# Kernel tuning notes

Measured on AMD Instinct MI355X. Metric: run time of the kernel, lower is better.

The kernel has to match this reference:

```python
import jax, jax.numpy as jnp
import numpy as np

RATIO = 2
GROUPS = 4


def conv1x1(x, w, b):
    # x: (B,C,H,W), w: (O,C), b: (O,)
    return jnp.einsum('bchw,oc->bohw', x, w) + b[None, :, None, None]


def pixel_unshuffle(x, r):
    # out[b, c*r*r + i*r + j, h, w] = x[b, c, h*r+i, w*r+j]  (torch semantics)
    B, C, H, W = x.shape
    x = x.reshape(B, C, H // r, r, W // r, r)
    x = x.transpose(0, 1, 3, 5, 2, 4)
    return x.reshape(B, C * r * r, H // r, W // r)


def grid_sample_bilinear_border(img, grid):
    # img: (N,C,H,W); grid: (N,Ho,Wo,2), grid[...,0]=x coord, grid[...,1]=y coord in [-1,1]
    # align_corners=False, padding_mode='border' (torch: clip coord to border, then bilinear)
    N, C, H, W = img.shape
    ix = ((grid[..., 0] + 1.0) * W - 1.0) * 0.5
    iy = ((grid[..., 1] + 1.0) * H - 1.0) * 0.5
    ix = jnp.clip(ix, 0.0, W - 1.0)
    iy = jnp.clip(iy, 0.0, H - 1.0)
    x0 = jnp.floor(ix)
    y0 = jnp.floor(iy)
    wx = (ix - x0)[:, None]  # (N,1,Ho,Wo) broadcast over C
    wy = (iy - y0)[:, None]
    x0i = x0.astype(jnp.int32)
    y0i = y0.astype(jnp.int32)
    x1i = jnp.minimum(x0i + 1, W - 1)
    y1i = jnp.minimum(y0i + 1, H - 1)
    gather = jax.vmap(lambda im, yy, xx: im[:, yy, xx])  # (C,Ho,Wo) per batch
    v00 = gather(img, y0i, x0i)
    v01 = gather(img, y0i, x1i)
    v10 = gather(img, y1i, x0i)
    v11 = gather(img, y1i, x1i)
    return (v00 * (1 - wx) * (1 - wy) + v01 * wx * (1 - wy)
            + v10 * (1 - wx) * wy + v11 * wx * wy)


def setup_inputs() -> dict:
    key = jax.random.key(0)
    k1, k2, k3 = jax.random.split(key, 3)
    B, C, H, W = 16, 64, 256, 256
    c_out = 2 * (GROUPS // RATIO ** 2)  # = 2
    x = jax.random.normal(k1, (B, C, H, W), jnp.float32)
    w_off = jax.random.normal(k2, (c_out, C), jnp.float32) * 0.001
    b_off = jnp.zeros((c_out,), jnp.float32)
    w_sc = jax.random.normal(k3, (c_out, C), jnp.float32) * 0.001
    b_sc = jnp.zeros((c_out,), jnp.float32)
    return {"x": x, "w_off": w_off, "b_off": b_off, "w_sc": w_sc, "b_sc": b_sc}


def reference(x, w_off, b_off, w_sc, b_sc):
    B, Cin, H, W = x.shape  # H,W divisible by RATIO -> replicate pad is a no-op
    # forward_lp with dyScope=True
    off = conv1x1(x, w_off, b_off)
    off = jax.nn.sigmoid(conv1x1(x, w_sc, b_sc)) * 0.5 * off
    off = pixel_unshuffle(off, RATIO)            # (B, 2*GROUPS, h, w)
    h, w = off.shape[2], off.shape[3]
    # x: 'b (c grp) h w -> (b grp) c h w'
    cg = Cin // GROUPS
    xg = x.reshape(B, cg, GROUPS, H, W).transpose(0, 2, 1, 3, 4).reshape(B * GROUPS, cg, H, W)
    # offset: 'b (grp two) h w -> (b grp) h w two'
    offg = off.reshape(B, GROUPS, 2, h, w).transpose(0, 1, 3, 4, 2).reshape(B * GROUPS, h, w, 2)
    # pos: stack(meshgrid(h_coord, w_coord)) -> channel 0 = h_coord, channel 1 = w_coord
    hc = jnp.arange(h, dtype=x.dtype) + 0.5
    wc = jnp.arange(w, dtype=x.dtype) + 0.5
    pos = jnp.stack(jnp.meshgrid(hc, wc, indexing='ij'), axis=-1)[None]  # (1,h,w,2)
    norm = jnp.array([w, h], dtype=x.dtype)  # normalizer = [w, h]
    grid = 2.0 * (pos + offg) / norm - 1.0
    out = grid_sample_bilinear_border(xg, grid)  # (B*GROUPS, cg, h, w)
    out = out.reshape(B, GROUPS, cg, h, w).transpose(0, 2, 1, 3, 4).reshape(B, Cin, h, w)
    return out, offg
```

## Files before the change

### kernel.cpp

```cpp
#include <hip/hip_runtime.h>
#include <math.h>

#define BATCH 16
#define CIN   64
#define HIN   256
#define WIN   256
#define HOUT  128
#define WOUT  128
#define NPIX  (HIN * WIN)
#define NPIXO (HOUT * WOUT)
#define OUT0_SIZE ((size_t)BATCH * CIN * HOUT * WOUT)

typedef __attribute__((ext_vector_type(4))) float f32x4;

__global__ __launch_bounds__(256) void k_fused(
    const float* __restrict__ x,
    const float* __restrict__ w_off, const float* __restrict__ b_off,
    const float* __restrict__ w_sc,  const float* __restrict__ b_sc,
    float* __restrict__ out, float* __restrict__ offg)
{
    __shared__ float  sw[256];
    __shared__ float2 soff[4][16][17];
    __shared__ __align__(16) float sval[5184];

    int t = threadIdx.x;
    sw[t] = (t < 128) ? w_off[t] : w_sc[t - 128];

    int blk  = blockIdx.x;
    int b    = blk >> 6;
    int tile = blk & 63;
    int hh0  = (tile >> 3) * 16;
    int ww0  = (tile & 7) * 16;

    int row = t >> 4, col = t & 15;
    int hh = hh0 + row, ww = ww0 + col;
    int odd = t & 1;
    int colbase = 2 * (ww0 + (col & 14));

    const float* xrow = x + (size_t)b * CIN * NPIX
                      + (size_t)(2 * hh + odd) * WIN + colbase;

    float TA0[4] = {0,0,0,0}, TA1[4] = {0,0,0,0};
    float TS0[4] = {0,0,0,0}, TS1[4] = {0,0,0,0};

    __syncthreads();

    #pragma unroll 8
    for (int c = 0; c < CIN; ++c) {
        f32x4 f = *reinterpret_cast<const f32x4*>(xrow + (size_t)c * NPIX);
        float wo0 = sw[c], wo1 = sw[64 + c], ws0 = sw[128 + c], ws1 = sw[192 + c];
        #pragma unroll
        for (int j = 0; j < 4; ++j) {
            TA0[j] += f[j] * wo0;
            TA1[j] += f[j] * wo1;
            TS0[j] += f[j] * ws0;
            TS1[j] += f[j] * ws1;
        }
    }

    float rA0_0 = __shfl_xor(odd ? TA0[0] : TA0[2], 1);
    float rA0_1 = __shfl_xor(odd ? TA0[1] : TA0[3], 1);
    float rA1_0 = __shfl_xor(odd ? TA1[0] : TA1[2], 1);
    float rA1_1 = __shfl_xor(odd ? TA1[1] : TA1[3], 1);
    float rS0_0 = __shfl_xor(odd ? TS0[0] : TS0[2], 1);
    float rS0_1 = __shfl_xor(odd ? TS0[1] : TS0[3], 1);
    float rS1_0 = __shfl_xor(odd ? TS1[0] : TS1[2], 1);
    float rS1_1 = __shfl_xor(odd ? TS1[1] : TS1[3], 1);

    float aA0[2][2], aA1[2][2], aS0[2][2], aS1[2][2];
    aA0[0][0] = odd ? rA0_0 : TA0[0];  aA0[0][1] = odd ? rA0_1 : TA0[1];
    aA0[1][0] = odd ? TA0[2] : rA0_0;  aA0[1][1] = odd ? TA0[3] : rA0_1;
    aA1[0][0] = odd ? rA1_0 : TA1[0];  aA1[0][1] = odd ? rA1_1 : TA1[1];
    aA1[1][0] = odd ? TA1[2] : rA1_0;  aA1[1][1] = odd ? TA1[3] : rA1_1;
    aS0[0][0] = odd ? rS0_0 : TS0[0];  aS0[0][1] = odd ? rS0_1 : TS0[1];
    aS0[1][0] = odd ? TS0[2] : rS0_0;  aS0[1][1] = odd ? TS0[3] : rS0_1;
    aS1[0][0] = odd ? rS1_0 : TS1[0];  aS1[0][1] = odd ? rS1_1 : TS1[1];
    aS1[1][0] = odd ? TS1[2] : rS1_0;  aS1[1][1] = odd ? TS1[3] : rS1_1;

    float bo0 = b_off[0], bo1 = b_off[1];
    float bs0 = b_sc[0],  bs1 = b_sc[1];

    float og[4][2];
    #pragma unroll
    for (int i = 0; i < 2; ++i) {
        #pragma unroll
        for (int j = 0; j < 2; ++j) {
            float g0 = 1.0f / (1.0f + __expf(-(aS0[i][j] + bs0)));
            float g1 = 1.0f / (1.0f + __expf(-(aS1[i][j] + bs1)));
            og[i][j]     = g0 * 0.5f * (aA0[i][j] + bo0);
            og[2 + i][j] = g1 * 0.5f * (aA1[i][j] + bo1);
        }
    }

    #pragma unroll
    for (int g = 0; g < 4; ++g) {
        float2 vv = make_float2(og[g][0], og[g][1]);
        soff[g][row][col] = vv;
        size_t oi = ((size_t)((b * 4 + g) * HOUT + hh)) * WOUT + ww;
        __builtin_nontemporal_store(__builtin_bit_cast(double, vv),
                                    reinterpret_cast<double*>(offg + 2 * oi));
    }
    __syncthreads();

    int hl = t & 15, wl = t >> 4;
    int shh = hh0 + hl, sww = ww0 + wl;
    int oddl = t & 1;
    const float* xg = x + (size_t)b * CIN * NPIX;

    int R  = (t >> 2) & 15;
    int q  = t & 3;
    int wv = t >> 6;

    float* outb = out + (size_t)b * CIN * NPIXO
                + (size_t)(hh0 + R) * WOUT + ww0 + q * 4;

    #pragma unroll
    for (int g = 0; g < 4; ++g) {
        float2 off = soff[g][hl][wl];
        float ix = 2.0f * ((float)shh + 0.5f + off.x) - 0.5f;
        float iy = 2.0f * ((float)sww + 0.5f + off.y) - 0.5f;
        ix = fminf(fmaxf(ix, 0.0f), (float)(WIN - 1));
        iy = fminf(fmaxf(iy, 0.0f), (float)(HIN - 1));

        float x0f = floorf(ix), y0f = floorf(iy);
        float wx = ix - x0f, wy = iy - y0f;
        int x0 = (int)x0f, y0 = (int)y0f;
        int x1 = min(x0 + 1, WIN - 1);
        int y1 = min(y0 + 1, HIN - 1);

        float w00 = (1.0f - wx) * (1.0f - wy);
        float w01 = wx * (1.0f - wy);
        float w10 = (1.0f - wx) * wy;
        float w11 = wx * wy;

        const float* xgc = xg + (size_t)g * NPIX;

        int x0p = __shfl_xor(x0, 1);
        int y0p = __shfl_xor(y0, 1);
        bool ok = (x1 == x0 + 1) && (y1 == y0 + 1) && (y0p == y0)
               && (oddl ? (x0 == x0p + 2) : (x0p == x0 + 2))
               && (((x0 - (oddl ? 2 : 0)) & 3) == 0);

        float v[16];
        if (__all(ok)) {
            int colb = x0 - (oddl ? 2 : 0);
            int rowL = oddl ? y1 : y0;
            float rw0 = __shfl_xor(oddl ? w00 : w10, 1);
            float rw1 = __shfl_xor(oddl ? w01 : w11, 1);
            const float* basep = xgc + (size_t)rowL * WIN + colb;
            #pragma unroll
            for (int c = 0; c < 16; ++c) {
                f32x4 f = *reinterpret_cast<const f32x4*>(basep + (size_t)c * 4 * NPIX);
                float pOwn  = oddl ? (f[2] * w10 + f[3] * w11)
                                   : (f[0] * w00 + f[1] * w01);
                float pPart = oddl ? (f[0] * rw0 + f[1] * rw1)
                                   : (f[2] * rw0 + f[3] * rw1);
                v[c] = pOwn + __shfl_xor(pPart, 1);
            }
        } else {
            int i00 = y0 * WIN + x0, i01 = y0 * WIN + x1;
            int i10 = y1 * WIN + x0, i11 = y1 * WIN + x1;
            bool fastp = ((x0 & 1) == 0) && (x1 == x0 + 1);
            if (fastp) {
                #pragma unroll
                for (int c = 0; c < 16; ++c) {
                    const float* xc = xgc + (size_t)c * 4 * NPIX;
                    float2 a = *reinterpret_cast<const float2*>(xc + i00);
                    float2 d = *reinterpret_cast<const float2*>(xc + i10);
                    v[c] = a.x * w00 + a.y * w01 + d.x * w10 + d.y * w11;
                }
            } else {
                #pragma unroll
                for (int c = 0; c < 16; ++c) {
                    const float* xc = xgc + (size_t)c * 4 * NPIX;
                    v[c] = xc[i00] * w00 + xc[i01] * w01
                         + xc[i10] * w10 + xc[i11] * w11;
                }
            }
        }

        __syncthreads();
        #pragma unroll
        for (int c = 0; c < 16; ++c)
            sval[c * 324 + hl * 20 + wl] = v[c];
        __syncthreads();

        #pragma unroll
        for (int p2 = 0; p2 < 4; ++p2) {
            int c = wv * 4 + p2;
            f32x4 val = *reinterpret_cast<const f32x4*>(&sval[c * 324 + R * 20 + q * 4]);
            __builtin_nontemporal_store(val, reinterpret_cast<f32x4*>(
                outb + (size_t)(c * 4 + g) * NPIXO));
        }
    }
}

extern "C" void kernel_launch(void* const* d_in, const int* in_sizes, int n_in,
                              void* d_out, int out_size, void* d_ws, size_t ws_size,
                              hipStream_t stream) {
    const float* x     = (const float*)d_in[0];
    const float* w_off = (const float*)d_in[1];
    const float* b_off = (const float*)d_in[2];
    const float* w_sc  = (const float*)d_in[3];
    const float* b_sc  = (const float*)d_in[4];

    float* out  = (float*)d_out;
    float* offg = out + OUT0_SIZE;

    k_fused<<<1024, 256, 0, stream>>>(x, w_off, b_off, w_sc, b_sc, out, offg);
}
```

Before: 100.6 us.

## Warp-specialize fused kernel into producer/consumer halves pipelining tiles

Each block now has 512 threads: 256 producer threads compute the offset convolution for the next tile while 256 consumer threads do grid-sample and write out the previous tile, with double-buffered shared memory for offsets and sampled values. The grid shrinks to 256 persistent-style blocks, each handling four tiles in sequence with a staggered tile order. The aim is to overlap the memory-bound conv pass with the gather pass and to spread the output stores across steps. In exchange it adds many block-wide barriers and drops to one block per CU, which lowers occupancy and latency hiding.

```diff
diff --git a/kernel.cpp b/kernel.cpp
--- a/kernel.cpp
+++ b/kernel.cpp
@@ -9,188 +9,237 @@
 #define WOUT  128
 #define NPIX  (HIN * WIN)
 #define NPIXO (HOUT * WOUT)
-#define OUT0_SIZE ((size_t)BATCH * CIN * HOUT * WOUT)
+#define OUT0_SIZE ((size_t)BATCH * CIN * NPIXO)
 
 typedef __attribute__((ext_vector_type(4))) float f32x4;
 
-__global__ __launch_bounds__(256) void k_fused(
+__global__ __launch_bounds__(512, 1) void k_fused(
     const float* __restrict__ x,
     const float* __restrict__ w_off, const float* __restrict__ b_off,
     const float* __restrict__ w_sc,  const float* __restrict__ b_sc,
     float* __restrict__ out, float* __restrict__ offg)
 {
     __shared__ float  sw[256];
-    __shared__ float2 soff[4][16][17];
-    __shared__ __align__(16) float sval[5184];
-
-    int t = threadIdx.x;
-    sw[t] = (t < 128) ? w_off[t] : w_sc[t - 128];
-
-    int blk  = blockIdx.x;
-    int b    = blk >> 6;
-    int tile = blk & 63;
-    int hh0  = (tile >> 3) * 16;
-    int ww0  = (tile & 7) * 16;
-
-    int row = t >> 4, col = t & 15;
-    int hh = hh0 + row, ww = ww0 + col;
-    int odd = t & 1;
-    int colbase = 2 * (ww0 + (col & 14));
-
-    const float* xrow = x + (size_t)b * CIN * NPIX
-                      + (size_t)(2 * hh + odd) * WIN + colbase;
-
-    float TA0[4] = {0,0,0,0}, TA1[4] = {0,0,0,0};
-    float TS0[4] = {0,0,0,0}, TS1[4] = {0,0,0,0};
+    __shared__ float2 soff[2][4][16][17];
+    __shared__ __align__(16) float sval[2][5184];
+
+    const int t = threadIdx.x;
+    if (t < 256) sw[t] = (t < 128) ? w_off[t] : w_sc[t - 128];
+
+    const int blk = blockIdx.x;
+    const int b   = blk >> 4;
+    const int k   = blk & 15;
+    const int pr  = k >> 1;
+    const int jj  = k & 1;
+    const int hh0 = pr * 16;
+
+    const bool isProd = (t < 256);
+    const int u = t & 255;
+
+    const int prow = u >> 4, pcol = u & 15;
+    const int phh  = hh0 + prow;
+    const int podd = u & 1;
+    const float* xbase = x + (size_t)b * CIN * NPIX
+                       + (size_t)(2 * phh + podd) * WIN;
+    float bo0 = 0, bo1 = 0, bs0 = 0, bs1 = 0;
+    if (isProd) { bo0 = b_off[0]; bo1 = b_off[1]; bs0 = b_sc[0]; bs1 = b_sc[1]; }
+
+    const int hl = u & 15, wl = u >> 4;
+    const int shh = hh0 + hl;
+    const int oddl = u & 1;
+    const float* xg = x + (size_t)b * CIN * NPIX;
+    const int Rr = (u >> 2) & 15, q4 = u & 3, wv = u >> 6;
+    float* outTB = out + (size_t)b * CIN * NPIXO
+                 + (size_t)(hh0 + Rr) * WOUT + q4 * 4;
+
+    int prev_ww0 = 0;
 
     __syncthreads();
 
-    #pragma unroll 8
-    for (int c = 0; c < CIN; ++c) {
-        f32x4 f = *reinterpret_cast<const f32x4*>(xrow + (size_t)c * NPIX);
-        float wo0 = sw[c], wo1 = sw[64 + c], ws0 = sw[128 + c], ws1 = sw[192 + c];
+    for (int r = 0; r < 5; ++r) {
+        const bool prodA = (r <= 3);
+        const bool consA = (r >= 1);
+        const int qp = ((r - pr) & 3) + 4 * jj;
+        const int qc = (((r - 1) - pr) & 3) + 4 * jj;
+        const int ww0p = qp * 16;
+        const int ww0c = qc * 16;
+
+        float TA0[4] = {0,0,0,0}, TA1[4] = {0,0,0,0};
+        float TS0[4] = {0,0,0,0}, TS1[4] = {0,0,0,0};
+
         #pragma unroll
-        for (int j = 0; j < 4; ++j) {
-            TA0[j] += f[j] * wo0;
-            TA1[j] += f[j] * wo1;
-            TS0[j] += f[j] * ws0;
-            TS1[j] += f[j] * ws1;
-        }
-    }
-
-    float rA0_0 = __shfl_xor(odd ? TA0[0] : TA0[2], 1);
-    float rA0_1 = __shfl_xor(odd ? TA0[1] : TA0[3], 1);
-    float rA1_0 = __shfl_xor(odd ? TA1[0] : TA1[2], 1);
-    float rA1_1 = __shfl_xor(odd ? TA1[1] : TA1[3], 1);
-    float rS0_0 = __shfl_xor(odd ? TS0[0] : TS0[2], 1);
-    float rS0_1 = __shfl_xor(odd ? TS0[1] : TS0[3], 1);
-    float rS1_0 = __shfl_xor(odd ? TS1[0] : TS1[2], 1);
-    float rS1_1 = __shfl_xor(odd ? TS1[1] : TS1[3], 1);
-
-    float aA0[2][2], aA1[2][2], aS0[2][2], aS1[2][2];
-    aA0[0][0] = odd ? rA0_0 : TA0[0];  aA0[0][1] = odd ? rA0_1 : TA0[1];
-    aA0[1][0] = odd ? TA0[2] : rA0_0;  aA0[1][1] = odd ? TA0[3] : rA0_1;
-    aA1[0][0] = odd ? rA1_0 : TA1[0];  aA1[0][1] = odd ? rA1_1 : TA1[1];
-    aA1[1][0] = odd ? TA1[2] : rA1_0;  aA1[1][1] = odd ? TA1[3] : rA1_1;
-    aS0[0][0] = odd ? rS0_0 : TS0[0];  aS0[0][1] = odd ? rS0_1 : TS0[1];
-    aS0[1][0] = odd ? TS0[2] : rS0_0;  aS0[1][1] = odd ? TS0[3] : rS0_1;
-    aS1[0][0] = odd ? rS1_0 : TS1[0];  aS1[0][1] = odd ? rS1_1 : TS1[1];
-    aS1[1][0] = odd ? TS1[2] : rS1_0;  aS1[1][1] = odd ? TS1[3] : rS1_1;
-
-    float bo0 = b_off[0], bo1 = b_off[1];
-    float bs0 = b_sc[0],  bs1 = b_sc[1];
-
-    float og[4][2];
-    #pragma unroll
-    for (int i = 0; i < 2; ++i) {
-        #pragma unroll
-        for (int j = 0; j < 2; ++j) {
-            float g0 = 1.0f / (1.0f + __expf(-(aS0[i][j] + bs0)));
-            float g1 = 1.0f / (1.0f + __expf(-(aS1[i][j] + bs1)));
-            og[i][j]     = g0 * 0.5f * (aA0[i][j] + bo0);
-            og[2 + i][j] = g1 * 0.5f * (aA1[i][j] + bo1);
-        }
-    }
-
-    #pragma unroll
-    for (int g = 0; g < 4; ++g) {
-        float2 vv = make_float2(og[g][0], og[g][1]);
-        soff[g][row][col] = vv;
-        size_t oi = ((size_t)((b * 4 + g) * HOUT + hh)) * WOUT + ww;
-        __builtin_nontemporal_store(__builtin_bit_cast(double, vv),
-                                    reinterpret_cast<double*>(offg + 2 * oi));
-    }
-    __syncthreads();
-
-    int hl = t & 15, wl = t >> 4;
-    int shh = hh0 + hl, sww = ww0 + wl;
-    int oddl = t & 1;
-    const float* xg = x + (size_t)b * CIN * NPIX;
-
-    int R  = (t >> 2) & 15;
-    int q  = t & 3;
-    int wv = t >> 6;
-
-    float* outb = out + (size_t)b * CIN * NPIXO
-                + (size_t)(hh0 + R) * WOUT + ww0 + q * 4;
-
-    #pragma unroll
-    for (int g = 0; g < 4; ++g) {
-        float2 off = soff[g][hl][wl];
-        float ix = 2.0f * ((float)shh + 0.5f + off.x) - 0.5f;
-        float iy = 2.0f * ((float)sww + 0.5f + off.y) - 0.5f;
-        ix = fminf(fmaxf(ix, 0.0f), (float)(WIN - 1));
-        iy = fminf(fmaxf(iy, 0.0f), (float)(HIN - 1));
-
-        float x0f = floorf(ix), y0f = floorf(iy);
-        float wx = ix - x0f, wy = iy - y0f;
-        int x0 = (int)x0f, y0 = (int)y0f;
-        int x1 = min(x0 + 1, WIN - 1);
-        int y1 = min(y0 + 1, HIN - 1);
-
-        float w00 = (1.0f - wx) * (1.0f - wy);
-        float w01 = wx * (1.0f - wy);
-        float w10 = (1.0f - wx) * wy;
-        float w11 = wx * wy;
-
-        const float* xgc = xg + (size_t)g * NPIX;
-
-        int x0p = __shfl_xor(x0, 1);
-        int y0p = __shfl_xor(y0, 1);
-        bool ok = (x1 == x0 + 1) && (y1 == y0 + 1) && (y0p == y0)
-               && (oddl ? (x0 == x0p + 2) : (x0p == x0 + 2))
-               && (((x0 - (oddl ? 2 : 0)) & 3) == 0);
-
-        float v[16];
-        if (__all(ok)) {
-            int colb = x0 - (oddl ? 2 : 0);
-            int rowL = oddl ? y1 : y0;
-            float rw0 = __shfl_xor(oddl ? w00 : w10, 1);
-            float rw1 = __shfl_xor(oddl ? w01 : w11, 1);
-            const float* basep = xgc + (size_t)rowL * WIN + colb;
-            #pragma unroll
-            for (int c = 0; c < 16; ++c) {
-                f32x4 f = *reinterpret_cast<const f32x4*>(basep + (size_t)c * 4 * NPIX);
-                float pOwn  = oddl ? (f[2] * w10 + f[3] * w11)
-                                   : (f[0] * w00 + f[1] * w01);
-                float pPart = oddl ? (f[0] * rw0 + f[1] * rw1)
-                                   : (f[2] * rw0 + f[3] * rw1);
-                v[c] = pOwn + __shfl_xor(pPart, 1);
-            }
-        } else {
-            int i00 = y0 * WIN + x0, i01 = y0 * WIN + x1;
-            int i10 = y1 * WIN + x0, i11 = y1 * WIN + x1;
-            bool fastp = ((x0 & 1) == 0) && (x1 == x0 + 1);
-            if (fastp) {
-                #pragma unroll
-                for (int c = 0; c < 16; ++c) {
-                    const float* xc = xgc + (size_t)c * 4 * NPIX;
-                    float2 a = *reinterpret_cast<const float2*>(xc + i00);
-                    float2 d = *reinterpret_cast<const float2*>(xc + i10);
-                    v[c] = a.x * w00 + a.y * w01 + d.x * w10 + d.y * w11;
+        for (int g = 0; g < 4; ++g) {
+            if (isProd) {
+                if (prodA) {
+                    const float* xrow = xbase + 2 * (ww0p + (pcol & 14));
+                    #pragma unroll
+                    for (int ci = 0; ci < 16; ++ci) {
+                        const int c = g * 16 + ci;
+                        f32x4 f = *reinterpret_cast<const f32x4*>(
+                            xrow + (size_t)c * NPIX);
+                        float wo0 = sw[c], wo1 = sw[64 + c];
+                        float ws0 = sw[128 + c], ws1 = sw[192 + c];
+                        #pragma unroll
+                        for (int jx = 0; jx < 4; ++jx) {
+                            TA0[jx] += f[jx] * wo0;
+                            TA1[jx] += f[jx] * wo1;
+                            TS0[jx] += f[jx] * ws0;
+                            TS1[jx] += f[jx] * ws1;
+                        }
+                    }
+                    if (g == 3) {
+                        float rA0_0 = __shfl_xor(podd ? TA0[0] : TA0[2], 1);
+                        float rA0_1 = __shfl_xor(podd ? TA0[1] : TA0[3], 1);
+                        float rA1_0 = __shfl_xor(podd ? TA1[0] : TA1[2], 1);
+                        float rA1_1 = __shfl_xor(podd ? TA1[1] : TA1[3], 1);
+                        float rS0_0 = __shfl_xor(podd ? TS0[0] : TS0[2], 1);
+                        float rS0_1 = __shfl_xor(podd ? TS0[1] : TS0[3], 1);
+                        float rS1_0 = __shfl_xor(podd ? TS1[0] : TS1[2], 1);
+                        float rS1_1 = __shfl_xor(podd ? TS1[1] : TS1[3], 1);
+
+                        float aA0[2][2], aA1[2][2], aS0[2][2], aS1[2][2];
+                        aA0[0][0] = podd ? rA0_0 : TA0[0];  aA0[0][1] = podd ? rA0_1 : TA0[1];
+                        aA0[1][0] = podd ? TA0[2] : rA0_0;  aA0[1][1] = podd ? TA0[3] : rA0_1;
+                        aA1[0][0] = podd ? rA1_0 : TA1[0];  aA1[0][1] = podd ? rA1_1 : TA1[1];
+                        aA1[1][0] = podd ? TA1[2] : rA1_0;  aA1[1][1] = podd ? TA1[3] : rA1_1;
+                        aS0[0][0] = podd ? rS0_0 : TS0[0];  aS0[0][1] = podd ? rS0_1 : TS0[1];
+                        aS0[1][0] = podd ? TS0[2] : rS0_0;  aS0[1][1] = podd ? TS0[3] : rS0_1;
+                        aS1[0][0] = podd ? rS1_0 : TS1[0];  aS1[0][1] = podd ? rS1_1 : TS1[1];
+                        aS1[1][0] = podd ? TS1[2] : rS1_0;  aS1[1][1] = podd ? TS1[3] : rS1_1;
+
+                        float og[4][2];
+                        #pragma unroll
+                        for (int i = 0; i < 2; ++i) {
+                            #pragma unroll
+                            for (int jy = 0; jy < 2; ++jy) {
+                                float g0 = 1.0f / (1.0f + __expf(-(aS0[i][jy] + bs0)));
+                                float g1 = 1.0f / (1.0f + __expf(-(aS1[i][jy] + bs1)));
+                                og[i][jy]     = g0 * 0.5f * (aA0[i][jy] + bo0);
+                                og[2 + i][jy] = g1 * 0.5f * (aA1[i][jy] + bo1);
+                            }
+                        }
+                        #pragma unroll
+                        for (int gg = 0; gg < 4; ++gg) {
+                            float2 vv = make_float2(og[gg][0], og[gg][1]);
+                            soff[r & 1][gg][prow][pcol] = vv;
+                            size_t oi = ((size_t)((b * 4 + gg) * HOUT + phh)) * WOUT
+                                      + (ww0p + pcol);
+                            __builtin_nontemporal_store(
+                                __builtin_bit_cast(double, vv),
+                                reinterpret_cast<double*>(offg + 2 * oi));
+                        }
+                    }
                 }
             } else {
-                #pragma unroll
-                for (int c = 0; c < 16; ++c) {
-                    const float* xc = xgc + (size_t)c * 4 * NPIX;
-                    v[c] = xc[i00] * w00 + xc[i01] * w01
-                         + xc[i10] * w10 + xc[i11] * w11;
+                if (consA) {
+                    if (g == 0) {
+                        if (r >= 2) {
+                            #pragma unroll
+                            for (int p2 = 0; p2 < 4; ++p2) {
+                                const int c = wv * 4 + p2;
+                                f32x4 val = *reinterpret_cast<const f32x4*>(
+                                    &sval[1][c * 324 + Rr * 20 + q4 * 4]);
+                                __builtin_nontemporal_store(val,
+                                    reinterpret_cast<f32x4*>(outTB + prev_ww0
+                                        + (size_t)(c * 4 + 3) * NPIXO));
+                            }
+                        }
+                    } else {
+                        #pragma unroll
+                        for (int p2 = 0; p2 < 4; ++p2) {
+                            const int c = wv * 4 + p2;
+                            f32x4 val = *reinterpret_cast<const f32x4*>(
+                                &sval[(g - 1) & 1][c * 324 + Rr * 20 + q4 * 4]);
+                            __builtin_nontemporal_store(val,
+                                reinterpret_cast<f32x4*>(outTB + ww0c
+                                    + (size_t)(c * 4 + (g - 1)) * NPIXO));
+                        }
+                    }
+
+                    float2 off = soff[(r - 1) & 1][g][hl][wl];
+                    const int sww = ww0c + wl;
+                    float ix = 2.0f * ((float)shh + 0.5f + off.x) - 0.5f;
+                    float iy = 2.0f * ((float)sww + 0.5f + off.y) - 0.5f;
+                    ix = fminf(fmaxf(ix, 0.0f), (float)(WIN - 1));
+                    iy = fminf(fmaxf(iy, 0.0f), (float)(HIN - 1));
+
+                    float x0f = floorf(ix), y0f = floorf(iy);
+                    float wx = ix - x0f, wy = iy - y0f;
+                    int x0 = (int)x0f, y0 = (int)y0f;
+                    int x1 = min(x0 + 1, WIN - 1);
+                    int y1 = min(y0 + 1, HIN - 1);
+
+                    float w00 = (1.0f - wx) * (1.0f - wy);
+                    float w01 = wx * (1.0f - wy);
+                    float w10 = (1.0f - wx) * wy;
+                    float w11 = wx * wy;
+
+                    const float* xgc = xg + (size_t)g * NPIX;
+
+                    int x0p = __shfl_xor(x0, 1);
+                    int y0p = __shfl_xor(y0, 1);
+                    bool ok = (x1 == x0 + 1) && (y1 == y0 + 1) && (y0p == y0)
+                           && (oddl ? (x0 == x0p + 2) : (x0p == x0 + 2))
+                           && (((x0 - (oddl ? 2 : 0)) & 3) == 0);
+
+                    float v[16];
+                    if (__all(ok)) {
+                        int colb = x0 - (oddl ? 2 : 0);
+                        int rowL = oddl ? y1 : y0;
+                        float rw0 = __shfl_xor(oddl ? w00 : w10, 1);
+                        float rw1 = __shfl_xor(oddl ? w01 : w11, 1);
+                        const float* basep = xgc + (size_t)rowL * WIN + colb;
+                        #pragma unroll
+                        for (int c = 0; c < 16; ++c) {
+                            f32x4 f = *reinterpret_cast<const f32x4*>(
+                                basep + (size_t)c * 4 * NPIX);
+                            float pOwn  = oddl ? (f[2] * w10 + f[3] * w11)
+                                               : (f[0] * w00 + f[1] * w01);
+                            float pPart = oddl ? (f[0] * rw0 + f[1] * rw1)
+                                               : (f[2] * rw0 + f[3] * rw1);
+                            v[c] = pOwn + __shfl_xor(pPart, 1);
+                        }
+                    } else {
+                        int i00 = y0 * WIN + x0, i01 = y0 * WIN + x1;
+                        int i10 = y1 * WIN + x0, i11 = y1 * WIN + x1;
+                        bool fastp = ((x0 & 1) == 0) && (x1 == x0 + 1);
+                        if (fastp) {
+                            #pragma unroll
+                            for (int c = 0; c < 16; ++c) {
+                                const float* xc = xgc + (size_t)c * 4 * NPIX;
+                                float2 a = *reinterpret_cast<const float2*>(xc + i00);
+                                float2 d = *reinterpret_cast<const float2*>(xc + i10);
+                                v[c] = a.x * w00 + a.y * w01 + d.x * w10 + d.y * w11;
+                            }
+                        } else {
+                            #pragma unroll
+                            for (int c = 0; c < 16; ++c) {
+                                const float* xc = xgc + (size_t)c * 4 * NPIX;
+                                v[c] = xc[i00] * w00 + xc[i01] * w01
+                                     + xc[i10] * w10 + xc[i11] * w11;
+                            }
+                        }
+                    }
+
+                    #pragma unroll
+                    for (int c = 0; c < 16; ++c)
+                        sval[g & 1][c * 324 + hl * 20 + wl] = v[c];
                 }
             }
+            __syncthreads();
         }
-
-        __syncthreads();
-        #pragma unroll
-        for (int c = 0; c < 16; ++c)
-            sval[c * 324 + hl * 20 + wl] = v[c];
-        __syncthreads();
-
+        if (!isProd && consA) prev_ww0 = ww0c;
+    }
+
+    if (!isProd) {
         #pragma unroll
         for (int p2 = 0; p2 < 4; ++p2) {
-            int c = wv * 4 + p2;
-            f32x4 val = *reinterpret_cast<const f32x4*>(&sval[c * 324 + R * 20 + q * 4]);
-            __builtin_nontemporal_store(val, reinterpret_cast<f32x4*>(
-                outb + (size_t)(c * 4 + g) * NPIXO));
+            const int c = wv * 4 + p2;
+            f32x4 val = *reinterpret_cast<const f32x4*>(
+                &sval[1][c * 324 + Rr * 20 + q4 * 4]);
+            __builtin_nontemporal_store(val,
+                reinterpret_cast<f32x4*>(outTB + prev_ww0
+                    + (size_t)(c * 4 + 3) * NPIXO));
         }
     }
 }
@@ -207,5 +256,5 @@
     float* out  = (float*)d_out;
     float* offg = out + OUT0_SIZE;
 
-    k_fused<<<1024, 256, 0, stream>>>(x, w_off, b_off, w_sc, b_sc, out, offg);
+    k_fused<<<256, 512, 0, stream>>>(x, w_off, b_off, w_sc, b_sc, out, offg);
 }
```

Measured after the change: 99.19 us. Within noise of the previous version (-1.4%).
